# Optimization experiments

Hardware: AMD Instinct MI355X
Metric: run time of the kernel (lower is better)

The kernel has to match this reference:

```python
import jax, jax.numpy as jnp
import numpy as np

N_JOB, N_SKILL = 100000, 20000
H, D = 4, 64            # heads, per-head dim (hidden_channels)
F_DIM = H * D           # 256 = heads * hidden_channels
IN = 256                # in_channels
E_SJ, E_JJ, E_JS = 500000, 500000, 250000


def setup_inputs() -> dict:
    key = jax.random.key(0)
    ks = jax.random.split(key, 24)
    rn = lambda k, s, sc=0.05: jax.random.normal(k, s, dtype=jnp.float32) * sc
    z = lambda s: jnp.zeros(s, jnp.float32)
    return dict(
        x_job=rn(ks[0], (N_JOB, IN), 1.0),
        x_skill=rn(ks[1], (N_SKILL, IN), 1.0),
        W_job=rn(ks[2], (IN, F_DIM)), b_job=z((F_DIM,)),
        W_skill=rn(ks[3], (IN, F_DIM)), b_skill=z((F_DIM,)),
        a_src_sj=rn(ks[4], (H, D)), a_dst_sj=rn(ks[5], (H, D)),
        a_src_jj=rn(ks[6], (H, D)), a_dst_jj=rn(ks[7], (H, D)),
        a_src_js=rn(ks[8], (H, D)), a_dst_js=rn(ks[9], (H, D)),
        q=rn(ks[10], (F_DIM,)), Wk=rn(ks[11], (F_DIM, F_DIM)), bk=z((F_DIM,)),
        W1=rn(ks[12], (F_DIM, F_DIM)), b1=z((F_DIM,)),
        W2=rn(ks[13], (F_DIM, 1)), b2=z((1,)),
        ei_sj_src=jax.random.randint(ks[14], (E_SJ,), 0, N_SKILL),
        ei_sj_dst=jax.random.randint(ks[15], (E_SJ,), 0, N_JOB),
        ei_jj_src=jax.random.randint(ks[16], (E_JJ,), 0, N_JOB),
        ei_jj_dst=jax.random.randint(ks[17], (E_JJ,), 0, N_JOB),
        ei_js_src=jax.random.randint(ks[18], (E_JS,), 0, N_JOB),
        ei_js_dst=jax.random.randint(ks[19], (E_JS,), 0, N_SKILL),
    )


def _gat(x_src, x_dst, a_src, a_dst, src, dst, n_dst):
    # x_src: [Ns,H,D], x_dst: [Nd,H,D]; GAT-style node-level attention per edge type.
    al = jnp.einsum('nhd,hd->nh', x_src, a_src)[src] + jnp.einsum('nhd,hd->nh', x_dst, a_dst)[dst]
    al = jax.nn.leaky_relu(al, 0.2)                      # [E,H]
    amax = jax.lax.stop_gradient(jax.ops.segment_max(al, dst, n_dst))
    e = jnp.exp(al - amax[dst])
    denom = jax.ops.segment_sum(e, dst, n_dst)
    alpha = e / (denom[dst] + 1e-16)                     # softmax over incoming edges per dst
    out = jax.ops.segment_sum(x_src[src] * alpha[:, :, None], dst, n_dst)  # [Nd,H,D]
    return jax.nn.relu(out.reshape(n_dst, H * D))


def _group(outs, q, Wk, bk):
    # semantic-level attention across edge types (shared q, k_lin)
    stk = jnp.stack(outs)                                # [M,N,F]
    score = jnp.einsum('f,mf->m', q, jnp.tanh(stk @ Wk + bk).mean(1))
    attn = jax.nn.softmax(score)
    return jnp.einsum('m,mnf->nf', attn, stk)


def reference(x_job, x_skill, W_job, b_job, W_skill, b_skill,
              a_src_sj, a_dst_sj, a_src_jj, a_dst_jj, a_src_js, a_dst_js,
              q, Wk, bk, W1, b1, W2, b2,
              ei_sj_src, ei_sj_dst, ei_jj_src, ei_jj_dst, ei_js_src, ei_js_dst):
    h_job = (x_job @ W_job + b_job).reshape(N_JOB, H, D)
    h_skill = (x_skill @ W_skill + b_skill).reshape(N_SKILL, H, D)
    out_sj = _gat(h_skill, h_job, a_src_sj, a_dst_sj, ei_sj_src, ei_sj_dst, N_JOB)
    out_jj = _gat(h_job, h_job, a_src_jj, a_dst_jj, ei_jj_src, ei_jj_dst, N_JOB)
    out_js = _gat(h_job, h_skill, a_src_js, a_dst_js, ei_js_src, ei_js_dst, N_SKILL)
    job = _group([out_sj, out_jj], q, Wk, bk)            # 'job' node type
    _ = _group([out_js], q, Wk, bk)                      # 'skill' node type (unused by head)
    # dropout is identity in eval mode; MLP head (mlp_layers=2)
    h = jax.nn.relu(job @ W1 + b1)
    return (h @ W2 + b2)[:, 0]
```

## Files before the change

kernel.cpp:

```cpp
#include <hip/hip_runtime.h>
#include <hip/hip_bf16.h>
#include <math.h>

#define SCAN_B 256
#define NEG_BIG (-3.0e38f)

typedef __attribute__((ext_vector_type(8))) short bf16x8;
typedef __attribute__((ext_vector_type(4))) float f32x4;

__device__ __forceinline__ unsigned short f2bf(float f) {
    __hip_bfloat16 h = __float2bfloat16(f);
    return *(unsigned short*)&h;
}
__device__ __forceinline__ float bf2f(unsigned short u) {
    unsigned v = ((unsigned)u) << 16;
    return __uint_as_float(v);
}
__device__ __forceinline__ float lrelu(float x) { return (x >= 0.f) ? x : 0.2f * x; }

__device__ __forceinline__ unsigned blend2(unsigned a, unsigned b, float c0, float c1) {
    float alo = bf2f((unsigned short)(a & 0xffff)), ahi = bf2f((unsigned short)(a >> 16));
    float blo = bf2f((unsigned short)(b & 0xffff)), bhi = bf2f((unsigned short)(b >> 16));
    unsigned short rlo = f2bf(c0 * alo + c1 * blo);
    unsigned short rhi = f2bf(c0 * ahi + c1 * bhi);
    return (unsigned)rlo | ((unsigned)rhi << 16);
}

template<int MODE, int NV>
__launch_bounds__(512)
__global__ void gemm_mfma(const unsigned short* __restrict__ Abf,
                          const unsigned short* __restrict__ A2bf,
                          const unsigned short* __restrict__ Bt,
                          const float* __restrict__ bias,
                          const float* __restrict__ vq,
                          const float* __restrict__ b2p,
                          const float* __restrict__ attn2,
                          unsigned short* __restrict__ outh,
                          float* __restrict__ outf,
                          float* __restrict__ scoreSlot,
                          const float* __restrict__ av0,
                          const float* __restrict__ av1,
                          const float* __restrict__ av2,
                          float* __restrict__ lo0,
                          float* __restrict__ lo1,
                          float* __restrict__ lo2,
                          int M)
{
    __shared__ __align__(16) char sm[49152];
    __shared__ float red8[8];
    const int t    = threadIdx.x;
    const int lane = t & 63, wid = t >> 6;
    const int wr = wid >> 2, wc = wid & 3;
    const long row0 = (long)blockIdx.x * 128;
    const char* Ab = (const char*)((MODE == 1 && blockIdx.y == 1) ? A2bf : Abf);
    const char* A2 = (const char*)A2bf;
    const char* Bb = (const char*)Bt;

    float blend0 = 0.f, blend1 = 0.f;
    if (MODE == 2) { blend0 = attn2[0]; blend1 = attn2[1]; }

    f32x4 acc[4][4];
#pragma unroll
    for (int m = 0; m < 4; ++m)
#pragma unroll
        for (int n = 0; n < 4; ++n) acc[m][n] = (f32x4){0.f, 0.f, 0.f, 0.f};

    for (int k0 = 0; k0 < 256; k0 += 64) {
#pragma unroll
        for (int rep = 0; rep < 2; ++rep) {
            int idx = rep * 512 + t;
            int row = idx >> 3, colb = (idx & 7) << 4;
            uint4 v = *(const uint4*)(Ab + (row0 + row) * 512 + k0 * 2 + colb);
            if (MODE == 2) {
                uint4 v2 = *(const uint4*)(A2 + (row0 + row) * 512 + k0 * 2 + colb);
                v.x = blend2(v.x, v2.x, blend0, blend1);
                v.y = blend2(v.y, v2.y, blend0, blend1);
                v.z = blend2(v.z, v2.z, blend0, blend1);
                v.w = blend2(v.w, v2.w, blend0, blend1);
            }
            *(uint4*)&sm[row * 128 + (colb ^ ((row & 7) << 4))] = v;
        }
#pragma unroll
        for (int rep = 0; rep < 4; ++rep) {
            int idx = rep * 512 + t;
            int n = idx >> 3, colb = (idx & 7) << 4;
            uint4 v = *(const uint4*)(Bb + n * 512 + k0 * 2 + colb);
            *(uint4*)&sm[16384 + n * 128 + (colb ^ ((n & 7) << 4))] = v;
        }
        __syncthreads();
#pragma unroll
        for (int kki = 0; kki < 2; ++kki) {
            const int kb = kki * 64 + ((lane >> 4) << 4);
            bf16x8 a[4], b[4];
#pragma unroll
            for (int m = 0; m < 4; ++m) {
                int row = wr * 64 + m * 16 + (lane & 15);
                a[m] = *(const bf16x8*)&sm[row * 128 + (kb ^ ((row & 7) << 4))];
            }
#pragma unroll
            for (int n = 0; n < 4; ++n) {
                int nr = wc * 64 + n * 16 + (lane & 15);
                b[n] = *(const bf16x8*)&sm[16384 + nr * 128 + (kb ^ ((nr & 7) << 4))];
            }
#pragma unroll
            for (int m = 0; m < 4; ++m)
#pragma unroll
                for (int n = 0; n < 4; ++n)
                    acc[m][n] = __builtin_amdgcn_mfma_f32_16x16x32_bf16(a[m], b[n], acc[m][n], 0, 0, 0);
        }
        __syncthreads();
    }

    const int colbase = wc * 64 + (lane & 15);
    const int rbase   = wr * 64 + ((lane >> 4) << 2);
    float bv[4];
#pragma unroll
    for (int n = 0; n < 4; ++n) bv[n] = bias[colbase + n * 16];

    if (MODE == 0) {
        float areg[(NV > 0) ? NV : 1][4];
#pragma unroll
        for (int v = 0; v < NV; ++v) {
            const float* av = (v == 0) ? av0 : (v == 1) ? av1 : av2;
#pragma unroll
            for (int n = 0; n < 4; ++n) areg[v][n] = av[colbase + n * 16];
        }
#pragma unroll
        for (int m = 0; m < 4; ++m) {
#pragma unroll
            for (int j = 0; j < 4; ++j) {
                long row = row0 + rbase + m * 16 + j;
                float hv[4];
#pragma unroll
                for (int n = 0; n < 4; ++n) hv[n] = acc[m][n][j] + bv[n];
                if (row < M) {
#pragma unroll
                    for (int n = 0; n < 4; ++n)
                        outh[row * 256 + colbase + n * 16] = f2bf(hv[n]);
                }
#pragma unroll
                for (int v = 0; v < NV; ++v) {
                    float p = hv[0] * areg[v][0] + hv[1] * areg[v][1]
                            + hv[2] * areg[v][2] + hv[3] * areg[v][3];
                    p += __shfl_xor(p, 1); p += __shfl_xor(p, 2);
                    p += __shfl_xor(p, 4); p += __shfl_xor(p, 8);
                    if ((lane & 15) == 0 && row < M) {
                        float* lo = (v == 0) ? lo0 : (v == 1) ? lo1 : lo2;
                        lo[row * 4 + wc] = p;
                    }
                }
            }
        }
    } else if (MODE == 1) {
        float p = 0.f;
        float qv[4];
#pragma unroll
        for (int n = 0; n < 4; ++n) qv[n] = vq[colbase + n * 16];
#pragma unroll
        for (int n = 0; n < 4; ++n) {
#pragma unroll
            for (int m = 0; m < 4; ++m) {
                long row = row0 + rbase + m * 16;
#pragma unroll
                for (int j = 0; j < 4; ++j)
                    if (row + j < M) p += qv[n] * tanhf(acc[m][n][j] + bv[n]);
            }
        }
#pragma unroll
        for (int off = 32; off > 0; off >>= 1) p += __shfl_xor(p, off);
        if (lane == 0) red8[wid] = p;
        __syncthreads();
        if (t == 0) {
            float s = 0.f;
#pragma unroll
            for (int i = 0; i < 8; ++i) s += red8[i];
            atomicAdd(&scoreSlot[blockIdx.y], s);
        }
    } else {
        float* redC = (float*)sm;
        float b2v = b2p[0];
        float wv[4];
#pragma unroll
        for (int n = 0; n < 4; ++n) wv[n] = vq[colbase + n * 16];
#pragma unroll
        for (int m = 0; m < 4; ++m) {
#pragma unroll
            for (int j = 0; j < 4; ++j) {
                float s = 0.f;
#pragma unroll
                for (int n = 0; n < 4; ++n)
                    s += fmaxf(acc[m][n][j] + bv[n], 0.f) * wv[n];
                s += __shfl_xor(s, 1); s += __shfl_xor(s, 2);
                s += __shfl_xor(s, 4); s += __shfl_xor(s, 8);
                if ((lane & 15) == 0) {
                    int lrow = wr * 64 + m * 16 + ((lane >> 4) << 2) + j;
                    redC[lrow * 4 + wc] = s;
                }
            }
        }
        __syncthreads();
        if (t < 128) {
            long row = row0 + t;
            if (row < M)
                outf[row] = redC[t * 4 + 0] + redC[t * 4 + 1]
                          + redC[t * 4 + 2] + redC[t * 4 + 3] + b2v;
        }
    }
}

__global__ void cast_pad(const float* __restrict__ src, unsigned short* __restrict__ dst,
                         long n, long npad)
{
    long i = ((long)blockIdx.x * 256 + threadIdx.x) * 4;
    if (i >= npad) return;
    ushort4 o;
    if (i + 4 <= n) {
        float4 v = *(const float4*)&src[i];
        o.x = f2bf(v.x); o.y = f2bf(v.y); o.z = f2bf(v.z); o.w = f2bf(v.w);
    } else {
        float vv[4];
#pragma unroll
        for (int j = 0; j < 4; ++j) vv[j] = (i + j < n) ? src[i + j] : 0.f;
        o.x = f2bf(vv[0]); o.y = f2bf(vv[1]); o.z = f2bf(vv[2]); o.w = f2bf(vv[3]);
    }
    *(ushort4*)&dst[i] = o;
}

__global__ void transpose_cast(const float* __restrict__ W, unsigned short* __restrict__ Wt)
{
    int n = blockIdx.x, k = threadIdx.x;
    Wt[n * 256 + k] = f2bf(W[k * 256 + n]);
}

__global__ void hist2(const int* __restrict__ d0, int E0, int* __restrict__ g0,
                      const int* __restrict__ d1, int E1, int* __restrict__ g1)
{
    int e = blockIdx.x * 256 + threadIdx.x;
    if (blockIdx.y == 0) { if (e < E0) atomicAdd(&g0[d0[e]], 1); }
    else                 { if (e < E1) atomicAdd(&g1[d1[e]], 1); }
}

__global__ void scan_bsum2(const int* __restrict__ g0, const int* __restrict__ g1, int n,
                           int* __restrict__ p0, int* __restrict__ p1)
{
    const int* deg = blockIdx.y ? g1 : g0;
    int* part      = blockIdx.y ? p1 : p0;
    __shared__ int smem[SCAN_B];
    int i = blockIdx.x * SCAN_B + threadIdx.x;
    smem[threadIdx.x] = (i < n) ? deg[i] : 0;
    __syncthreads();
    for (int off = SCAN_B / 2; off > 0; off >>= 1) {
        if (threadIdx.x < off) smem[threadIdx.x] += smem[threadIdx.x + off];
        __syncthreads();
    }
    if (threadIdx.x == 0) part[blockIdx.x] = smem[0];
}

__global__ void scan_part2(int* __restrict__ p0, int* __restrict__ p1, int nb)
{
    int* part = blockIdx.y ? p1 : p0;
    __shared__ int smem[1024];
    int t = threadIdx.x;
    int v = (t < nb) ? part[t] : 0;
    smem[t] = v;
    __syncthreads();
    for (int off = 1; off < 1024; off <<= 1) {
        int add = (t >= off) ? smem[t - off] : 0;
        __syncthreads();
        smem[t] += add;
        __syncthreads();
    }
    if (t < nb) part[t] = smem[t] - v;
}

__global__ void scan_final2(const int* __restrict__ g0, const int* __restrict__ g1, int n,
                            const int* __restrict__ p0, const int* __restrict__ p1,
                            int* __restrict__ r0, int* __restrict__ r1, int E0, int E1)
{
    const int* deg = blockIdx.y ? g1 : g0;
    const int* part = blockIdx.y ? p1 : p0;
    int* rowptr = blockIdx.y ? r1 : r0;
    int E = blockIdx.y ? E1 : E0;
    __shared__ int smem[SCAN_B];
    int t = threadIdx.x;
    int i = blockIdx.x * SCAN_B + t;
    int v = (i < n) ? deg[i] : 0;
    smem[t] = v;
    __syncthreads();
    for (int off = 1; off < SCAN_B; off <<= 1) {
        int add = (t >= off) ? smem[t - off] : 0;
        __syncthreads();
        smem[t] += add;
        __syncthreads();
    }
    if (i < n) rowptr[i] = part[blockIdx.x] + smem[t] - v;
    if (blockIdx.x == 0 && t == 0) rowptr[n] = E;
}

__global__ void fill_csr2(const int* __restrict__ d0, int E0, const int* __restrict__ r0,
                          int* __restrict__ c0, int* __restrict__ o0,
                          const int* __restrict__ d1, int E1, const int* __restrict__ r1,
                          int* __restrict__ c1, int* __restrict__ o1)
{
    int e = blockIdx.x * 256 + threadIdx.x;
    if (blockIdx.y == 0) {
        if (e < E0) { int d = d0[e]; int s = atomicAdd(&c0[d], 1); o0[r0[d] + s] = e; }
    } else {
        if (e < E1) { int d = d1[e]; int s = atomicAdd(&c1[d], 1); o1[r1[d] + s] = e; }
    }
}

__launch_bounds__(256)
__global__ void gat_fused(const unsigned short* __restrict__ xs0,
                          const unsigned short* __restrict__ xs1,
                          const float* __restrict__ als0, const float* __restrict__ als1,
                          const float* __restrict__ ald0, const float* __restrict__ ald1,
                          const int* __restrict__ rp0, const int* __restrict__ rp1,
                          const int* __restrict__ csr0, const int* __restrict__ csr1,
                          const int* __restrict__ src0, const int* __restrict__ src1,
                          int N,
                          unsigned short* __restrict__ out0,
                          unsigned short* __restrict__ out1)
{
    const int et = blockIdx.y;
    const unsigned short* xsrc = et ? xs1 : xs0;
    const float* als = et ? als1 : als0;
    const float* ald = et ? ald1 : ald0;
    const int* rowptr = et ? rp1 : rp0;
    const int* csr    = et ? csr1 : csr0;
    const int* src    = et ? src1 : src0;
    unsigned short* outb = et ? out1 : out0;

    __shared__ float lw[4][64 * 4];
    __shared__ int   ls[4][64];
    const int wv   = threadIdx.x >> 6;
    const int w    = (int)((blockIdx.x * 256 + threadIdx.x) >> 6);
    const int lane = threadIdx.x & 63;
    if (w >= N) return;
    const int beg = rowptr[w], end = rowptr[w + 1];
    const int deg = end - beg;
    const int h = lane >> 4;
    const float4 d4 = *(const float4*)&ald[(size_t)w * 4];
    const size_t loff = (size_t)(lane << 2);

    float4 accA = make_float4(0.f, 0.f, 0.f, 0.f);
    float4 accB = make_float4(0.f, 0.f, 0.f, 0.f);
    float dn0 = 0.f, dn1 = 0.f, dn2 = 0.f, dn3 = 0.f;

    if (deg <= 64) {
        float al0 = NEG_BIG, al1 = NEG_BIG, al2 = NEG_BIG, al3 = NEG_BIG;
        int es = 0;
        if (lane < deg) {
            int e = csr[beg + lane];
            es = src[e];
            float4 a = *(const float4*)&als[(size_t)es * 4];
            al0 = lrelu(a.x + d4.x); al1 = lrelu(a.y + d4.y);
            al2 = lrelu(a.z + d4.z); al3 = lrelu(a.w + d4.w);
        }
        float m0 = al0, m1 = al1, m2 = al2, m3 = al3;
#pragma unroll
        for (int off = 32; off > 0; off >>= 1) {
            m0 = fmaxf(m0, __shfl_xor(m0, off));
            m1 = fmaxf(m1, __shfl_xor(m1, off));
            m2 = fmaxf(m2, __shfl_xor(m2, off));
            m3 = fmaxf(m3, __shfl_xor(m3, off));
        }
        float w0 = 0.f, w1 = 0.f, w2 = 0.f, w3 = 0.f;
        if (lane < deg) {
            w0 = expf(al0 - m0); w1 = expf(al1 - m1);
            w2 = expf(al2 - m2); w3 = expf(al3 - m3);
            ls[wv][lane] = es;
            lw[wv][lane * 4 + 0] = w0; lw[wv][lane * 4 + 1] = w1;
            lw[wv][lane * 4 + 2] = w2; lw[wv][lane * 4 + 3] = w3;
        }
        dn0 = w0; dn1 = w1; dn2 = w2; dn3 = w3;

        int i = 0;
        for (; i + 4 <= deg; i += 4) {
            int s0 = ls[wv][i + 0], s1 = ls[wv][i + 1];
            int s2 = ls[wv][i + 2], s3 = ls[wv][i + 3];
            float wx0 = lw[wv][(i + 0) * 4 + h], wx1 = lw[wv][(i + 1) * 4 + h];
            float wx2 = lw[wv][(i + 2) * 4 + h], wx3 = lw[wv][(i + 3) * 4 + h];
            ushort4 x0 = *(const ushort4*)&xsrc[(size_t)s0 * 256 + loff];
            ushort4 x1 = *(const ushort4*)&xsrc[(size_t)s1 * 256 + loff];
            ushort4 x2 = *(const ushort4*)&xsrc[(size_t)s2 * 256 + loff];
            ushort4 x3 = *(const ushort4*)&xsrc[(size_t)s3 * 256 + loff];
            accA.x += wx0 * bf2f(x0.x); accA.y += wx0 * bf2f(x0.y);
            accA.z += wx0 * bf2f(x0.z); accA.w += wx0 * bf2f(x0.w);
            accB.x += wx1 * bf2f(x1.x); accB.y += wx1 * bf2f(x1.y);
            accB.z += wx1 * bf2f(x1.z); accB.w += wx1 * bf2f(x1.w);
            accA.x += wx2 * bf2f(x2.x); accA.y += wx2 * bf2f(x2.y);
            accA.z += wx2 * bf2f(x2.z); accA.w += wx2 * bf2f(x2.w);
            accB.x += wx3 * bf2f(x3.x); accB.y += wx3 * bf2f(x3.y);
            accB.z += wx3 * bf2f(x3.z); accB.w += wx3 * bf2f(x3.w);
        }
        for (; i < deg; ++i) {
            int s = ls[wv][i];
            float wx = lw[wv][i * 4 + h];
            ushort4 xu = *(const ushort4*)&xsrc[(size_t)s * 256 + loff];
            accA.x += wx * bf2f(xu.x); accA.y += wx * bf2f(xu.y);
            accA.z += wx * bf2f(xu.z); accA.w += wx * bf2f(xu.w);
        }
    } else {
        float m0 = NEG_BIG, m1 = NEG_BIG, m2 = NEG_BIG, m3 = NEG_BIG;
        for (int c = beg; c < end; c += 64) {
            if (c + lane < end) {
                int e = csr[c + lane];
                int s = src[e];
                float4 a = *(const float4*)&als[(size_t)s * 4];
                m0 = fmaxf(m0, lrelu(a.x + d4.x)); m1 = fmaxf(m1, lrelu(a.y + d4.y));
                m2 = fmaxf(m2, lrelu(a.z + d4.z)); m3 = fmaxf(m3, lrelu(a.w + d4.w));
            }
        }
#pragma unroll
        for (int off = 32; off > 0; off >>= 1) {
            m0 = fmaxf(m0, __shfl_xor(m0, off));
            m1 = fmaxf(m1, __shfl_xor(m1, off));
            m2 = fmaxf(m2, __shfl_xor(m2, off));
            m3 = fmaxf(m3, __shfl_xor(m3, off));
        }
        for (int c = beg; c < end; c += 64) {
            int cnt = min(64, end - c);
            if (lane < cnt) {
                int e = csr[c + lane];
                int es = src[e];
                float4 a = *(const float4*)&als[(size_t)es * 4];
                float w0 = expf(lrelu(a.x + d4.x) - m0);
                float w1 = expf(lrelu(a.y + d4.y) - m1);
                float w2 = expf(lrelu(a.z + d4.z) - m2);
                float w3 = expf(lrelu(a.w + d4.w) - m3);
                ls[wv][lane] = es;
                lw[wv][lane * 4 + 0] = w0; lw[wv][lane * 4 + 1] = w1;
                lw[wv][lane * 4 + 2] = w2; lw[wv][lane * 4 + 3] = w3;
                dn0 += w0; dn1 += w1; dn2 += w2; dn3 += w3;
            }
            int i = 0;
            for (; i + 4 <= cnt; i += 4) {
                int s0 = ls[wv][i + 0], s1 = ls[wv][i + 1];
                int s2 = ls[wv][i + 2], s3 = ls[wv][i + 3];
                float wx0 = lw[wv][(i + 0) * 4 + h], wx1 = lw[wv][(i + 1) * 4 + h];
                float wx2 = lw[wv][(i + 2) * 4 + h], wx3 = lw[wv][(i + 3) * 4 + h];
                ushort4 x0 = *(const ushort4*)&xsrc[(size_t)s0 * 256 + loff];
                ushort4 x1 = *(const ushort4*)&xsrc[(size_t)s1 * 256 + loff];
                ushort4 x2 = *(const ushort4*)&xsrc[(size_t)s2 * 256 + loff];
                ushort4 x3 = *(const ushort4*)&xsrc[(size_t)s3 * 256 + loff];
                accA.x += wx0 * bf2f(x0.x); accA.y += wx0 * bf2f(x0.y);
                accA.z += wx0 * bf2f(x0.z); accA.w += wx0 * bf2f(x0.w);
                accB.x += wx1 * bf2f(x1.x); accB.y += wx1 * bf2f(x1.y);
                accB.z += wx1 * bf2f(x1.z); accB.w += wx1 * bf2f(x1.w);
                accA.x += wx2 * bf2f(x2.x); accA.y += wx2 * bf2f(x2.y);
                accA.z += wx2 * bf2f(x2.z); accA.w += wx2 * bf2f(x2.w);
                accB.x += wx3 * bf2f(x3.x); accB.y += wx3 * bf2f(x3.y);
                accB.z += wx3 * bf2f(x3.z); accB.w += wx3 * bf2f(x3.w);
            }
            for (; i < cnt; ++i) {
                int s = ls[wv][i];
                float wx = lw[wv][i * 4 + h];
                ushort4 xu = *(const ushort4*)&xsrc[(size_t)s * 256 + loff];
                accA.x += wx * bf2f(xu.x); accA.y += wx * bf2f(xu.y);
                accA.z += wx * bf2f(xu.z); accA.w += wx * bf2f(xu.w);
            }
        }
    }

    float4 acc = make_float4(accA.x + accB.x, accA.y + accB.y,
                             accA.z + accB.z, accA.w + accB.w);
#pragma unroll
    for (int off = 32; off > 0; off >>= 1) {
        dn0 += __shfl_xor(dn0, off);
        dn1 += __shfl_xor(dn1, off);
        dn2 += __shfl_xor(dn2, off);
        dn3 += __shfl_xor(dn3, off);
    }
    float dh = (h == 0) ? dn0 : (h == 1) ? dn1 : (h == 2) ? dn2 : dn3;
    float inv = 1.f / (dh + 1e-16f);
    ushort4 uo;
    uo.x = f2bf(fmaxf(acc.x * inv, 0.f));
    uo.y = f2bf(fmaxf(acc.y * inv, 0.f));
    uo.z = f2bf(fmaxf(acc.z * inv, 0.f));
    uo.w = f2bf(fmaxf(acc.w * inv, 0.f));
    *(ushort4*)&outb[(size_t)w * 256 + loff] = uo;
}

__global__ void attn_k(const float* __restrict__ score, float* __restrict__ attn, float invN)
{
    if (threadIdx.x == 0 && blockIdx.x == 0) {
        float s0 = score[0] * invN, s1 = score[1] * invN;
        float m  = fmaxf(s0, s1);
        float e0 = expf(s0 - m), e1 = expf(s1 - m);
        float dsum = e0 + e1;
        attn[0] = e0 / dsum;
        attn[1] = e1 / dsum;
    }
}

extern "C" void kernel_launch(void* const* d_in, const int* in_sizes, int n_in,
                              void* d_out, int out_size, void* d_ws, size_t ws_size,
                              hipStream_t stream)
{
    const float* x_job    = (const float*)d_in[0];
    const float* x_skill  = (const float*)d_in[1];
    const float* W_job    = (const float*)d_in[2];
    const float* b_job    = (const float*)d_in[3];
    const float* W_skill  = (const float*)d_in[4];
    const float* b_skill  = (const float*)d_in[5];
    const float* a_src_sj = (const float*)d_in[6];
    const float* a_dst_sj = (const float*)d_in[7];
    const float* a_src_jj = (const float*)d_in[8];
    const float* a_dst_jj = (const float*)d_in[9];
    const float* q_vec = (const float*)d_in[12];
    const float* Wk    = (const float*)d_in[13];
    const float* bk    = (const float*)d_in[14];
    const float* W1    = (const float*)d_in[15];
    const float* b1    = (const float*)d_in[16];
    const float* W2    = (const float*)d_in[17];
    const float* b2    = (const float*)d_in[18];
    const int* ei_sj_src = (const int*)d_in[19];
    const int* ei_sj_dst = (const int*)d_in[20];
    const int* ei_jj_src = (const int*)d_in[21];
    const int* ei_jj_dst = (const int*)d_in[22];

    const int NJ   = in_sizes[0] / 256;
    const int NS   = in_sizes[1] / 256;
    const int E_sj = in_sizes[19];
    const int E_jj = in_sizes[21];
    const int Emax = (E_sj > E_jj) ? E_sj : E_jj;
    const int gmJ  = (NJ + 127) / 128, gmS = (NS + 127) / 128;
    const long MpadJ = (long)gmJ * 128, MpadS = (long)gmS * 128;

    char* ws   = (char*)d_ws;
    size_t off = 0;
    auto alloc = [&](size_t bytes) { void* p = ws + off; off += (bytes + 255) & ~(size_t)255; return p; };
    unsigned short* h_job_bf   = (unsigned short*)alloc(MpadJ * 256 * 2);
    unsigned short* h_skill_bf = (unsigned short*)alloc(MpadS * 256 * 2);
    unsigned short* x_job_bf   = (unsigned short*)alloc(MpadJ * 256 * 2);
    unsigned short* x_skill_bf = (unsigned short*)alloc(MpadS * 256 * 2);
    unsigned short* Wjob_t  = (unsigned short*)alloc(256 * 256 * 2);
    unsigned short* Wskl_t  = (unsigned short*)alloc(256 * 256 * 2);
    unsigned short* Wk_t    = (unsigned short*)alloc(256 * 256 * 2);
    unsigned short* W1_t    = (unsigned short*)alloc(256 * 256 * 2);
    unsigned short* out_sj_bf = (unsigned short*)alloc(MpadJ * 256 * 2);
    unsigned short* out_jj_bf = (unsigned short*)alloc(MpadJ * 256 * 2);
    float* ald_sj  = (float*)alloc((size_t)NJ * 4 * 4);
    float* als_jj  = (float*)alloc((size_t)NJ * 4 * 4);
    float* ald_jj  = (float*)alloc((size_t)NJ * 4 * 4);
    float* als_sj  = (float*)alloc((size_t)NS * 4 * 4);
    float* score  = (float*)alloc(64 * 4);
    float* attn   = score + 2;
    int* deg_sj = (int*)alloc((size_t)NJ * 4);
    int* deg_jj = (int*)alloc((size_t)NJ * 4);
    int* rp_sj  = (int*)alloc(((size_t)NJ + 1) * 4);
    int* rp_jj  = (int*)alloc(((size_t)NJ + 1) * 4);
    int* part_a = (int*)alloc(1024 * 4);
    int* part_b = (int*)alloc(1024 * 4);
    int* cur_sj = (int*)alloc((size_t)NJ * 4);
    int* cur_jj = (int*)alloc((size_t)NJ * 4);
    int* csr_sj = (int*)alloc((size_t)E_sj * 4);
    int* csr_jj = (int*)alloc((size_t)E_jj * 4);
    (void)ws_size; (void)n_in;

    hipMemsetAsync(score,  0, 2 * 4, stream);
    hipMemsetAsync(deg_sj, 0, (size_t)NJ * 4, stream);
    hipMemsetAsync(deg_jj, 0, (size_t)NJ * 4, stream);
    hipMemsetAsync(cur_sj, 0, (size_t)NJ * 4, stream);
    hipMemsetAsync(cur_jj, 0, (size_t)NJ * 4, stream);

    dim3 blk(256);
    int nbJ = (NJ + SCAN_B - 1) / SCAN_B;

    long nJ = (long)NJ * 256, nJp = MpadJ * 256;
    long nS = (long)NS * 256, nSp = MpadS * 256;
    cast_pad<<<dim3((int)((nJp / 4 + 255) / 256)), blk, 0, stream>>>(x_job, x_job_bf, nJ, nJp);
    cast_pad<<<dim3((int)((nSp / 4 + 255) / 256)), blk, 0, stream>>>(x_skill, x_skill_bf, nS, nSp);
    transpose_cast<<<dim3(256), blk, 0, stream>>>(W_job, Wjob_t);
    transpose_cast<<<dim3(256), blk, 0, stream>>>(W_skill, Wskl_t);
    transpose_cast<<<dim3(256), blk, 0, stream>>>(Wk, Wk_t);
    transpose_cast<<<dim3(256), blk, 0, stream>>>(W1, W1_t);

    hist2<<<dim3((Emax + 255) / 256, 2), blk, 0, stream>>>(
        ei_sj_dst, E_sj, deg_sj, ei_jj_dst, E_jj, deg_jj);
    scan_bsum2<<<dim3(nbJ, 2), dim3(SCAN_B), 0, stream>>>(deg_sj, deg_jj, NJ, part_a, part_b);
    scan_part2<<<dim3(1, 2), dim3(1024), 0, stream>>>(part_a, part_b, nbJ);
    scan_final2<<<dim3(nbJ, 2), dim3(SCAN_B), 0, stream>>>(
        deg_sj, deg_jj, NJ, part_a, part_b, rp_sj, rp_jj, E_sj, E_jj);
    fill_csr2<<<dim3((Emax + 255) / 256, 2), blk, 0, stream>>>(
        ei_sj_dst, E_sj, rp_sj, cur_sj, csr_sj,
        ei_jj_dst, E_jj, rp_jj, cur_jj, csr_jj);

    gemm_mfma<0, 3><<<dim3(gmJ), dim3(512), 0, stream>>>(
        x_job_bf, nullptr, Wjob_t, b_job, nullptr, nullptr, nullptr,
        h_job_bf, nullptr, nullptr,
        a_dst_sj, a_src_jj, a_dst_jj, ald_sj, als_jj, ald_jj, NJ);
    gemm_mfma<0, 1><<<dim3(gmS), dim3(512), 0, stream>>>(
        x_skill_bf, nullptr, Wskl_t, b_skill, nullptr, nullptr, nullptr,
        h_skill_bf, nullptr, nullptr,
        a_src_sj, nullptr, nullptr, als_sj, nullptr, nullptr, NS);

    gat_fused<<<dim3((NJ + 3) / 4, 2), blk, 0, stream>>>(
        h_skill_bf, h_job_bf, als_sj, als_jj, ald_sj, ald_jj,
        rp_sj, rp_jj, csr_sj, csr_jj, ei_sj_src, ei_jj_src, NJ,
        out_sj_bf, out_jj_bf);

    gemm_mfma<1, 0><<<dim3(gmJ, 2), dim3(512), 0, stream>>>(
        out_sj_bf, out_jj_bf, Wk_t, bk, q_vec, nullptr, nullptr,
        nullptr, nullptr, score,
        nullptr, nullptr, nullptr, nullptr, nullptr, nullptr, NJ);
    attn_k<<<1, 64, 0, stream>>>(score, attn, 1.0f / (float)NJ);

    gemm_mfma<2, 0><<<dim3(gmJ), dim3(512), 0, stream>>>(
        out_sj_bf, out_jj_bf, W1_t, b1, W2, b2, attn,
        nullptr, (float*)d_out, nullptr,
        nullptr, nullptr, nullptr, nullptr, nullptr, nullptr, NJ);
}
```

Baseline: 470.1 us.

## Fuse fp32-to-bf16 input cast into GEMM loads and widen GAT gathers

The first two GEMMs now read fp32 node features directly and convert them to bf16 while staging into shared memory. This removes the separate cast_pad kernels and their bf16 intermediate buffers, saving a full write and re-read of the inputs. The four weight transpose-cast launches are merged into one kernel. The GAT aggregation now has each half-wave gather 16-byte rows for a different edge, combined with a cross-half shuffle at the end, so each load instruction fetches more bytes; the cost is more registers and a shuffle reduction per node.

Result: no change. 466.6 us (-0.7%).

```diff
diff --git a/kernel.cpp b/kernel.cpp
--- a/kernel.cpp
+++ b/kernel.cpp
@@ -26,9 +26,21 @@
     return (unsigned)rlo | ((unsigned)rhi << 16);
 }
 
-template<int MODE, int NV>
+__device__ __forceinline__ void fma8(float* a, uint4 u, float w) {
+    a[0] += w * __uint_as_float(u.x << 16);
+    a[1] += w * __uint_as_float(u.x & 0xffff0000u);
+    a[2] += w * __uint_as_float(u.y << 16);
+    a[3] += w * __uint_as_float(u.y & 0xffff0000u);
+    a[4] += w * __uint_as_float(u.z << 16);
+    a[5] += w * __uint_as_float(u.z & 0xffff0000u);
+    a[6] += w * __uint_as_float(u.w << 16);
+    a[7] += w * __uint_as_float(u.w & 0xffff0000u);
+}
+
+template<int MODE, int NV, int AF32>
 __launch_bounds__(512)
-__global__ void gemm_mfma(const unsigned short* __restrict__ Abf,
+__global__ void gemm_mfma(const float* __restrict__ Af32,
+                          const unsigned short* __restrict__ Abf,
                           const unsigned short* __restrict__ A2bf,
                           const unsigned short* __restrict__ Bt,
                           const float* __restrict__ bias,
@@ -70,13 +82,29 @@
         for (int rep = 0; rep < 2; ++rep) {
             int idx = rep * 512 + t;
             int row = idx >> 3, colb = (idx & 7) << 4;
-            uint4 v = *(const uint4*)(Ab + (row0 + row) * 512 + k0 * 2 + colb);
-            if (MODE == 2) {
-                uint4 v2 = *(const uint4*)(A2 + (row0 + row) * 512 + k0 * 2 + colb);
-                v.x = blend2(v.x, v2.x, blend0, blend1);
-                v.y = blend2(v.y, v2.y, blend0, blend1);
-                v.z = blend2(v.z, v2.z, blend0, blend1);
-                v.w = blend2(v.w, v2.w, blend0, blend1);
+            uint4 v;
+            if (AF32) {
+                long grow = row0 + row;
+                if (grow < M) {
+                    const float* sp = Af32 + grow * 256 + k0 + ((idx & 7) << 3);
+                    float4 f0 = *(const float4*)sp;
+                    float4 f1 = *(const float4*)(sp + 4);
+                    v.x = (unsigned)f2bf(f0.x) | ((unsigned)f2bf(f0.y) << 16);
+                    v.y = (unsigned)f2bf(f0.z) | ((unsigned)f2bf(f0.w) << 16);
+                    v.z = (unsigned)f2bf(f1.x) | ((unsigned)f2bf(f1.y) << 16);
+                    v.w = (unsigned)f2bf(f1.z) | ((unsigned)f2bf(f1.w) << 16);
+                } else {
+                    v = make_uint4(0u, 0u, 0u, 0u);
+                }
+            } else {
+                v = *(const uint4*)(Ab + (row0 + row) * 512 + k0 * 2 + colb);
+                if (MODE == 2) {
+                    uint4 v2 = *(const uint4*)(A2 + (row0 + row) * 512 + k0 * 2 + colb);
+                    v.x = blend2(v.x, v2.x, blend0, blend1);
+                    v.y = blend2(v.y, v2.y, blend0, blend1);
+                    v.z = blend2(v.z, v2.z, blend0, blend1);
+                    v.w = blend2(v.w, v2.w, blend0, blend1);
+                }
             }
             *(uint4*)&sm[row * 128 + (colb ^ ((row & 7) << 4))] = v;
         }
@@ -208,28 +236,15 @@
     }
 }
 
-__global__ void cast_pad(const float* __restrict__ src, unsigned short* __restrict__ dst,
-                         long n, long npad)
-{
-    long i = ((long)blockIdx.x * 256 + threadIdx.x) * 4;
-    if (i >= npad) return;
-    ushort4 o;
-    if (i + 4 <= n) {
-        float4 v = *(const float4*)&src[i];
-        o.x = f2bf(v.x); o.y = f2bf(v.y); o.z = f2bf(v.z); o.w = f2bf(v.w);
-    } else {
-        float vv[4];
-#pragma unroll
-        for (int j = 0; j < 4; ++j) vv[j] = (i + j < n) ? src[i + j] : 0.f;
-        o.x = f2bf(vv[0]); o.y = f2bf(vv[1]); o.z = f2bf(vv[2]); o.w = f2bf(vv[3]);
-    }
-    *(ushort4*)&dst[i] = o;
-}
-
-__global__ void transpose_cast(const float* __restrict__ W, unsigned short* __restrict__ Wt)
-{
+__global__ void transpose_cast4(const float* __restrict__ W0, const float* __restrict__ W1s,
+                                const float* __restrict__ W2s, const float* __restrict__ W3s,
+                                unsigned short* __restrict__ T0, unsigned short* __restrict__ T1,
+                                unsigned short* __restrict__ T2, unsigned short* __restrict__ T3)
+{
+    const float* W = (blockIdx.y == 0) ? W0 : (blockIdx.y == 1) ? W1s : (blockIdx.y == 2) ? W2s : W3s;
+    unsigned short* T = (blockIdx.y == 0) ? T0 : (blockIdx.y == 1) ? T1 : (blockIdx.y == 2) ? T2 : T3;
     int n = blockIdx.x, k = threadIdx.x;
-    Wt[n * 256 + k] = f2bf(W[k * 256 + n]);
+    T[n * 256 + k] = f2bf(W[k * 256 + n]);
 }
 
 __global__ void hist2(const int* __restrict__ d0, int E0, int* __restrict__ g0,
@@ -339,12 +354,13 @@
     if (w >= N) return;
     const int beg = rowptr[w], end = rowptr[w + 1];
     const int deg = end - beg;
-    const int h = lane >> 4;
+    const int sub = lane & 31, half = lane >> 5;
+    const int h2 = sub >> 3;
     const float4 d4 = *(const float4*)&ald[(size_t)w * 4];
-    const size_t loff = (size_t)(lane << 2);
-
-    float4 accA = make_float4(0.f, 0.f, 0.f, 0.f);
-    float4 accB = make_float4(0.f, 0.f, 0.f, 0.f);
+    const size_t loff8 = (size_t)(sub << 3);
+
+    float a8A[8] = {0.f, 0.f, 0.f, 0.f, 0.f, 0.f, 0.f, 0.f};
+    float a8B[8] = {0.f, 0.f, 0.f, 0.f, 0.f, 0.f, 0.f, 0.f};
     float dn0 = 0.f, dn1 = 0.f, dn2 = 0.f, dn3 = 0.f;
 
     if (deg <= 64) {
@@ -377,29 +393,27 @@
 
         int i = 0;
         for (; i + 4 <= deg; i += 4) {
-            int s0 = ls[wv][i + 0], s1 = ls[wv][i + 1];
-            int s2 = ls[wv][i + 2], s3 = ls[wv][i + 3];
-            float wx0 = lw[wv][(i + 0) * 4 + h], wx1 = lw[wv][(i + 1) * 4 + h];
-            float wx2 = lw[wv][(i + 2) * 4 + h], wx3 = lw[wv][(i + 3) * 4 + h];
-            ushort4 x0 = *(const ushort4*)&xsrc[(size_t)s0 * 256 + loff];
-            ushort4 x1 = *(const ushort4*)&xsrc[(size_t)s1 * 256 + loff];
-            ushort4 x2 = *(const ushort4*)&xsrc[(size_t)s2 * 256 + loff];
-            ushort4 x3 = *(const ushort4*)&xsrc[(size_t)s3 * 256 + loff];
-            accA.x += wx0 * bf2f(x0.x); accA.y += wx0 * bf2f(x0.y);
-            accA.z += wx0 * bf2f(x0.z); accA.w += wx0 * bf2f(x0.w);
-            accB.x += wx1 * bf2f(x1.x); accB.y += wx1 * bf2f(x1.y);
-            accB.z += wx1 * bf2f(x1.z); accB.w += wx1 * bf2f(x1.w);
-            accA.x += wx2 * bf2f(x2.x); accA.y += wx2 * bf2f(x2.y);
-            accA.z += wx2 * bf2f(x2.z); accA.w += wx2 * bf2f(x2.w);
-            accB.x += wx3 * bf2f(x3.x); accB.y += wx3 * bf2f(x3.y);
-            accB.z += wx3 * bf2f(x3.z); accB.w += wx3 * bf2f(x3.w);
-        }
-        for (; i < deg; ++i) {
-            int s = ls[wv][i];
-            float wx = lw[wv][i * 4 + h];
-            ushort4 xu = *(const ushort4*)&xsrc[(size_t)s * 256 + loff];
-            accA.x += wx * bf2f(xu.x); accA.y += wx * bf2f(xu.y);
-            accA.z += wx * bf2f(xu.z); accA.w += wx * bf2f(xu.w);
+            int eA = i + half, eB = i + 2 + half;
+            int sA = ls[wv][eA], sB = ls[wv][eB];
+            float wA = lw[wv][eA * 4 + h2], wB = lw[wv][eB * 4 + h2];
+            uint4 xA = *(const uint4*)&xsrc[(size_t)sA * 256 + loff8];
+            uint4 xB = *(const uint4*)&xsrc[(size_t)sB * 256 + loff8];
+            fma8(a8A, xA, wA);
+            fma8(a8B, xB, wB);
+        }
+        if (i + 2 <= deg) {
+            int eA = i + half;
+            int sA = ls[wv][eA];
+            float wA = lw[wv][eA * 4 + h2];
+            uint4 xA = *(const uint4*)&xsrc[(size_t)sA * 256 + loff8];
+            fma8(a8A, xA, wA);
+            i += 2;
+        }
+        if (i < deg) {
+            int sA = ls[wv][i];
+            float wA = half ? 0.f : lw[wv][i * 4 + h2];
+            uint4 xA = *(const uint4*)&xsrc[(size_t)sA * 256 + loff8];
+            fma8(a8A, xA, wA);
         }
     } else {
         float m0 = NEG_BIG, m1 = NEG_BIG, m2 = NEG_BIG, m3 = NEG_BIG;
@@ -436,35 +450,36 @@
             }
             int i = 0;
             for (; i + 4 <= cnt; i += 4) {
-                int s0 = ls[wv][i + 0], s1 = ls[wv][i + 1];
-                int s2 = ls[wv][i + 2], s3 = ls[wv][i + 3];
-                float wx0 = lw[wv][(i + 0) * 4 + h], wx1 = lw[wv][(i + 1) * 4 + h];
-                float wx2 = lw[wv][(i + 2) * 4 + h], wx3 = lw[wv][(i + 3) * 4 + h];
-                ushort4 x0 = *(const ushort4*)&xsrc[(size_t)s0 * 256 + loff];
-                ushort4 x1 = *(const ushort4*)&xsrc[(size_t)s1 * 256 + loff];
-                ushort4 x2 = *(const ushort4*)&xsrc[(size_t)s2 * 256 + loff];
-                ushort4 x3 = *(const ushort4*)&xsrc[(size_t)s3 * 256 + loff];
-                accA.x += wx0 * bf2f(x0.x); accA.y += wx0 * bf2f(x0.y);
-                accA.z += wx0 * bf2f(x0.z); accA.w += wx0 * bf2f(x0.w);
-                accB.x += wx1 * bf2f(x1.x); accB.y += wx1 * bf2f(x1.y);
-                accB.z += wx1 * bf2f(x1.z); accB.w += wx1 * bf2f(x1.w);
-                accA.x += wx2 * bf2f(x2.x); accA.y += wx2 * bf2f(x2.y);
-                accA.z += wx2 * bf2f(x2.z); accA.w += wx2 * bf2f(x2.w);
-                accB.x += wx3 * bf2f(x3.x); accB.y += wx3 * bf2f(x3.y);
-                accB.z += wx3 * bf2f(x3.z); accB.w += wx3 * bf2f(x3.w);
-            }
-            for (; i < cnt; ++i) {
-                int s = ls[wv][i];
-                float wx = lw[wv][i * 4 + h];
-                ushort4 xu = *(const ushort4*)&xsrc[(size_t)s * 256 + loff];
-                accA.x += wx * bf2f(xu.x); accA.y += wx * bf2f(xu.y);
-                accA.z += wx * bf2f(xu.z); accA.w += wx * bf2f(xu.w);
-            }
-        }
-    }
-
-    float4 acc = make_float4(accA.x + accB.x, accA.y + accB.y,
-                             accA.z + accB.z, accA.w + accB.w);
+                int eA = i + half, eB = i + 2 + half;
+                int sA = ls[wv][eA], sB = ls[wv][eB];
+                float wA = lw[wv][eA * 4 + h2], wB = lw[wv][eB * 4 + h2];
+                uint4 xA = *(const uint4*)&xsrc[(size_t)sA * 256 + loff8];
+                uint4 xB = *(const uint4*)&xsrc[(size_t)sB * 256 + loff8];
+                fma8(a8A, xA, wA);
+                fma8(a8B, xB, wB);
+            }
+            if (i + 2 <= cnt) {
+                int eA = i + half;
+                int sA = ls[wv][eA];
+                float wA = lw[wv][eA * 4 + h2];
+                uint4 xA = *(const uint4*)&xsrc[(size_t)sA * 256 + loff8];
+                fma8(a8A, xA, wA);
+                i += 2;
+            }
+            if (i < cnt) {
+                int sA = ls[wv][i];
+                float wA = half ? 0.f : lw[wv][i * 4 + h2];
+                uint4 xA = *(const uint4*)&xsrc[(size_t)sA * 256 + loff8];
+                fma8(a8A, xA, wA);
+            }
+        }
+    }
+
+#pragma unroll
+    for (int j = 0; j < 8; ++j) a8A[j] += a8B[j];
+#pragma unroll
+    for (int j = 0; j < 8; ++j) a8A[j] += __shfl_xor(a8A[j], 32);
+
 #pragma unroll
     for (int off = 32; off > 0; off >>= 1) {
         dn0 += __shfl_xor(dn0, off);
@@ -472,14 +487,16 @@
         dn2 += __shfl_xor(dn2, off);
         dn3 += __shfl_xor(dn3, off);
     }
-    float dh = (h == 0) ? dn0 : (h == 1) ? dn1 : (h == 2) ? dn2 : dn3;
+    float dh = (h2 == 0) ? dn0 : (h2 == 1) ? dn1 : (h2 == 2) ? dn2 : dn3;
     float inv = 1.f / (dh + 1e-16f);
-    ushort4 uo;
-    uo.x = f2bf(fmaxf(acc.x * inv, 0.f));
-    uo.y = f2bf(fmaxf(acc.y * inv, 0.f));
-    uo.z = f2bf(fmaxf(acc.z * inv, 0.f));
-    uo.w = f2bf(fmaxf(acc.w * inv, 0.f));
-    *(ushort4*)&outb[(size_t)w * 256 + loff] = uo;
+    if (half == 0) {
+        uint4 o;
+        o.x = (unsigned)f2bf(fmaxf(a8A[0] * inv, 0.f)) | ((unsigned)f2bf(fmaxf(a8A[1] * inv, 0.f)) << 16);
+        o.y = (unsigned)f2bf(fmaxf(a8A[2] * inv, 0.f)) | ((unsigned)f2bf(fmaxf(a8A[3] * inv, 0.f)) << 16);
+        o.z = (unsigned)f2bf(fmaxf(a8A[4] * inv, 0.f)) | ((unsigned)f2bf(fmaxf(a8A[5] * inv, 0.f)) << 16);
+        o.w = (unsigned)f2bf(fmaxf(a8A[6] * inv, 0.f)) | ((unsigned)f2bf(fmaxf(a8A[7] * inv, 0.f)) << 16);
+        *(uint4*)&outb[(size_t)w * 256 + loff8] = o;
+    }
 }
 
 __global__ void attn_k(const float* __restrict__ score, float* __restrict__ attn, float invN)
@@ -533,8 +550,6 @@
     auto alloc = [&](size_t bytes) { void* p = ws + off; off += (bytes + 255) & ~(size_t)255; return p; };
     unsigned short* h_job_bf   = (unsigned short*)alloc(MpadJ * 256 * 2);
     unsigned short* h_skill_bf = (unsigned short*)alloc(MpadS * 256 * 2);
-    unsigned short* x_job_bf   = (unsigned short*)alloc(MpadJ * 256 * 2);
-    unsigned short* x_skill_bf = (unsigned short*)alloc(MpadS * 256 * 2);
     unsigned short* Wjob_t  = (unsigned short*)alloc(256 * 256 * 2);
     unsigned short* Wskl_t  = (unsigned short*)alloc(256 * 256 * 2);
     unsigned short* Wk_t    = (unsigned short*)alloc(256 * 256 * 2);
@@ -568,14 +583,8 @@
     dim3 blk(256);
     int nbJ = (NJ + SCAN_B - 1) / SCAN_B;
 
-    long nJ = (long)NJ * 256, nJp = MpadJ * 256;
-    long nS = (long)NS * 256, nSp = MpadS * 256;
-    cast_pad<<<dim3((int)((nJp / 4 + 255) / 256)), blk, 0, stream>>>(x_job, x_job_bf, nJ, nJp);
-    cast_pad<<<dim3((int)((nSp / 4 + 255) / 256)), blk, 0, stream>>>(x_skill, x_skill_bf, nS, nSp);
-    transpose_cast<<<dim3(256), blk, 0, stream>>>(W_job, Wjob_t);
-    transpose_cast<<<dim3(256), blk, 0, stream>>>(W_skill, Wskl_t);
-    transpose_cast<<<dim3(256), blk, 0, stream>>>(Wk, Wk_t);
-    transpose_cast<<<dim3(256), blk, 0, stream>>>(W1, W1_t);
+    transpose_cast4<<<dim3(256, 4), blk, 0, stream>>>(
+        W_job, W_skill, Wk, W1, Wjob_t, Wskl_t, Wk_t, W1_t);
 
     hist2<<<dim3((Emax + 255) / 256, 2), blk, 0, stream>>>(
         ei_sj_dst, E_sj, deg_sj, ei_jj_dst, E_jj, deg_jj);
@@ -587,12 +596,12 @@
         ei_sj_dst, E_sj, rp_sj, cur_sj, csr_sj,
         ei_jj_dst, E_jj, rp_jj, cur_jj, csr_jj);
 
-    gemm_mfma<0, 3><<<dim3(gmJ), dim3(512), 0, stream>>>(
-        x_job_bf, nullptr, Wjob_t, b_job, nullptr, nullptr, nullptr,
+    gemm_mfma<0, 3, 1><<<dim3(gmJ), dim3(512), 0, stream>>>(
+        x_job, nullptr, nullptr, Wjob_t, b_job, nullptr, nullptr, nullptr,
         h_job_bf, nullptr, nullptr,
         a_dst_sj, a_src_jj, a_dst_jj, ald_sj, als_jj, ald_jj, NJ);
-    gemm_mfma<0, 1><<<dim3(gmS), dim3(512), 0, stream>>>(
-        x_skill_bf, nullptr, Wskl_t, b_skill, nullptr, nullptr, nullptr,
+    gemm_mfma<0, 1, 1><<<dim3(gmS), dim3(512), 0, stream>>>(
+        x_skill, nullptr, nullptr, Wskl_t, b_skill, nullptr, nullptr, nullptr,
         h_skill_bf, nullptr, nullptr,
         a_src_sj, nullptr, nullptr, als_sj, nullptr, nullptr, NS);
 
@@ -601,14 +610,14 @@
         rp_sj, rp_jj, csr_sj, csr_jj, ei_sj_src, ei_jj_src, NJ,
         out_sj_bf, out_jj_bf);
 
-    gemm_mfma<1, 0><<<dim3(gmJ, 2), dim3(512), 0, stream>>>(
-        out_sj_bf, out_jj_bf, Wk_t, bk, q_vec, nullptr, nullptr,
+    gemm_mfma<1, 0, 0><<<dim3(gmJ, 2), dim3(512), 0, stream>>>(
+        nullptr, out_sj_bf, out_jj_bf, Wk_t, bk, q_vec, nullptr, nullptr,
         nullptr, nullptr, score,
         nullptr, nullptr, nullptr, nullptr, nullptr, nullptr, NJ);
     attn_k<<<1, 64, 0, stream>>>(score, attn, 1.0f / (float)NJ);
 
-    gemm_mfma<2, 0><<<dim3(gmJ), dim3(512), 0, stream>>>(
-        out_sj_bf, out_jj_bf, W1_t, b1, W2, b2, attn,
+    gemm_mfma<2, 0, 0><<<dim3(gmJ), dim3(512), 0, stream>>>(
+        nullptr, out_sj_bf, out_jj_bf, W1_t, b1, W2, b2, attn,
         nullptr, (float*)d_out, nullptr,
         nullptr, nullptr, nullptr, nullptr, nullptr, nullptr, NJ);
 }
```
